# Performance work log

Measured on AMD Instinct MI355X. Metric: run time of the kernel, lower is better.

## Reference

```python
import jax, jax.numpy as jnp
import numpy as np

B, N, DIM = 4, 2048, 512
HEADS, DIM_HEAD = 8, 64
INNER = HEADS * DIM_HEAD  # 512
EPS = 1e-5
SCALE = DIM_HEAD ** -0.5


def _layernorm(x, g):
    # matches custom LayerNorm: unbiased=False var, no bias term
    mean = jnp.mean(x, axis=-1, keepdims=True)
    var = jnp.var(x, axis=-1, keepdims=True)
    return (x - mean) * jax.lax.rsqrt(var + EPS) * g


def setup_inputs() -> dict:
    key = jax.random.key(0)
    ks = jax.random.split(key, 6)
    x = jax.random.normal(ks[0], (B, N, DIM), dtype=jnp.float32)
    attn_bias = jax.random.normal(ks[1], (HEADS, N, N), dtype=jnp.float32)
    w_q = jax.random.normal(ks[2], (DIM, INNER), dtype=jnp.float32) * 0.02
    w_kv = jax.random.normal(ks[3], (DIM, 2 * DIM_HEAD), dtype=jnp.float32) * 0.02
    w_out = jax.random.normal(ks[4], (INNER, DIM), dtype=jnp.float32) * 0.02
    g_in = jnp.ones((DIM,), dtype=jnp.float32)
    g_out = jnp.ones((DIM,), dtype=jnp.float32)
    return {"x": x, "attn_bias": attn_bias, "w_q": w_q, "w_kv": w_kv,
            "w_out": w_out, "g_in": g_in, "g_out": g_out}


def reference(x, attn_bias, w_q, w_kv, w_out, g_in, g_out):
    b, n, _ = x.shape
    xn = _layernorm(x, g_in)                                  # [b, n, dim]
    q = (xn @ w_q).reshape(b, n, HEADS, DIM_HEAD)
    q = jnp.transpose(q, (0, 2, 1, 3)) * SCALE                # [b, h, n, d]
    kv = xn @ w_kv                                            # [b, n, 2d]
    k, v = jnp.split(kv, 2, axis=-1)                          # each [b, n, d] (multi-query)
    sim = jnp.einsum('bhid,bjd->bhij', q, k) + attn_bias      # [b, h, n, n]
    attn = jax.nn.softmax(sim, axis=-1)
    out = jnp.einsum('bhij,bjd->bhid', attn, v)               # [b, h, n, d]
    out = jnp.transpose(out, (0, 2, 1, 3)).reshape(b, n, INNER)
    out = out @ w_out                                         # [b, n, dim]
    return _layernorm(out, g_out)
```

## Files before the change

### kernel.cpp

```cpp
#include <hip/hip_runtime.h>
#include <hip/hip_bf16.h>

#define B_ 4
#define N_ 2048
#define DIM_ 512
#define HEADS_ 8
#define DHEAD_ 64
#define EPS_ 1e-5f
#define SCALE_ 0.125f

typedef __attribute__((ext_vector_type(8))) short short8;
typedef __attribute__((ext_vector_type(4))) float f32x4;
#define MFMA16(a, b, c) __builtin_amdgcn_mfma_f32_16x16x32_bf16(a, b, c, 0, 0, 0)

__device__ __forceinline__ float bf2f(__hip_bfloat16 v) { return __bfloat162float(v); }
__device__ __forceinline__ float load_in(const void* p, size_t i, int isf32) {
    if (isf32) return ((const float*)p)[i];
    return bf2f(((const __hip_bfloat16*)p)[i]);
}

__global__ void detect_kernel(const unsigned int* __restrict__ g, int* __restrict__ flag) {
    if (threadIdx.x == 0 && blockIdx.x == 0)
        *flag = (*g == 0x3F800000u) ? 1 : 0;
}

__global__ __launch_bounds__(256) void transpose_w(const void* __restrict__ w,
                                                   __hip_bfloat16* __restrict__ wt,
                                                   int K, int N, const int* __restrict__ flag) {
    int isf32 = *flag;
    int idx = blockIdx.x * 256 + threadIdx.x;
    if (idx >= K * N) return;
    int k = idx / N, n = idx % N;
    wt[(size_t)n * K + k] = __float2bfloat16(load_in(w, idx, isf32));
}

__global__ __launch_bounds__(256) void ln1_kernel(const void* __restrict__ x,
                                                  const void* __restrict__ g,
                                                  __hip_bfloat16* __restrict__ out,
                                                  const int* __restrict__ flag) {
    int isf32 = *flag;
    int row = blockIdx.x;
    int tid = threadIdx.x;
    size_t base = (size_t)row * DIM_;
    float v0 = load_in(x, base + tid, isf32);
    float v1 = load_in(x, base + tid + 256, isf32);
    float s = v0 + v1;
    float sq = v0 * v0 + v1 * v1;
    for (int off = 32; off > 0; off >>= 1) {
        s += __shfl_xor(s, off, 64);
        sq += __shfl_xor(sq, off, 64);
    }
    __shared__ float ls[4], lq[4];
    int wid = tid >> 6;
    if ((tid & 63) == 0) { ls[wid] = s; lq[wid] = sq; }
    __syncthreads();
    s = ls[0] + ls[1] + ls[2] + ls[3];
    sq = lq[0] + lq[1] + lq[2] + lq[3];
    float mean = s * (1.0f / DIM_);
    float var = sq * (1.0f / DIM_) - mean * mean;
    float rstd = rsqrtf(var + EPS_);
    out[base + tid]       = __float2bfloat16((v0 - mean) * rstd * load_in(g, tid, isf32));
    out[base + tid + 256] = __float2bfloat16((v1 - mean) * rstd * load_in(g, tid + 256, isf32));
}

__global__ __launch_bounds__(256) void ln2_kernel(const float* __restrict__ x,
                                                  const void* __restrict__ g,
                                                  void* __restrict__ out,
                                                  const int* __restrict__ flag) {
    int isf32 = *flag;
    int row = blockIdx.x;
    int tid = threadIdx.x;
    const float* xr = x + (size_t)row * DIM_;
    float v0 = xr[tid];
    float v1 = xr[tid + 256];
    float s = v0 + v1;
    float sq = v0 * v0 + v1 * v1;
    for (int off = 32; off > 0; off >>= 1) {
        s += __shfl_xor(s, off, 64);
        sq += __shfl_xor(sq, off, 64);
    }
    __shared__ float ls[4], lq[4];
    int wid = tid >> 6;
    if ((tid & 63) == 0) { ls[wid] = s; lq[wid] = sq; }
    __syncthreads();
    s = ls[0] + ls[1] + ls[2] + ls[3];
    sq = lq[0] + lq[1] + lq[2] + lq[3];
    float mean = s * (1.0f / DIM_);
    float var = sq * (1.0f / DIM_) - mean * mean;
    float rstd = rsqrtf(var + EPS_);
    float r0 = (v0 - mean) * rstd * load_in(g, tid, isf32);
    float r1 = (v1 - mean) * rstd * load_in(g, tid + 256, isf32);
    size_t base = (size_t)row * DIM_;
    if (isf32) {
        ((float*)out)[base + tid] = r0;
        ((float*)out)[base + tid + 256] = r1;
    } else {
        ((__hip_bfloat16*)out)[base + tid] = __float2bfloat16(r0);
        ((__hip_bfloat16*)out)[base + tid + 256] = __float2bfloat16(r1);
    }
}

template <int MODE>
__global__ __launch_bounds__(256) void gemm_mfma(const __hip_bfloat16* __restrict__ A,
                                                 const __hip_bfloat16* __restrict__ Bt,
                                                 void* __restrict__ Cout,
                                                 void* __restrict__ Cout2,
                                                 int M, int N, int K) {
    __shared__ __align__(16) __hip_bfloat16 As[64][72];
    __shared__ __align__(16) __hip_bfloat16 Bs[64][72];
    int tid = threadIdx.x;
    int lane = tid & 63, wave = tid >> 6;
    int quad = lane >> 4, l15 = lane & 15;
    int wr = (wave & 1) * 32, wc = (wave >> 1) * 32;
    int m0 = blockIdx.y * 64, n0 = blockIdx.x * 64;
    f32x4 acc[2][2] = {};

    for (int k0 = 0; k0 < K; k0 += 64) {
        __syncthreads();
#pragma unroll
        for (int t = 0; t < 2; ++t) {
            int idx = tid + 256 * t;
            int r = idx >> 3, cc = (idx & 7) * 8;
            *(uint4*)&As[r][cc] = *(const uint4*)(A + (size_t)(m0 + r) * K + k0 + cc);
            *(uint4*)&Bs[r][cc] = *(const uint4*)(Bt + (size_t)(n0 + r) * K + k0 + cc);
        }
        __syncthreads();
#pragma unroll
        for (int ks = 0; ks < 2; ++ks) {
            short8 a0 = *(const short8*)&As[wr + l15][ks * 32 + quad * 8];
            short8 a1 = *(const short8*)&As[wr + 16 + l15][ks * 32 + quad * 8];
            short8 b0 = *(const short8*)&Bs[wc + l15][ks * 32 + quad * 8];
            short8 b1 = *(const short8*)&Bs[wc + 16 + l15][ks * 32 + quad * 8];
            acc[0][0] = MFMA16(a0, b0, acc[0][0]);
            acc[0][1] = MFMA16(a0, b1, acc[0][1]);
            acc[1][0] = MFMA16(a1, b0, acc[1][0]);
            acc[1][1] = MFMA16(a1, b1, acc[1][1]);
        }
    }
#pragma unroll
    for (int i = 0; i < 2; ++i)
#pragma unroll
        for (int j = 0; j < 2; ++j)
#pragma unroll
            for (int r = 0; r < 4; ++r) {
                int row = m0 + wr + i * 16 + quad * 4 + r;
                int col = n0 + wc + j * 16 + l15;
                float v = acc[i][j][r];
                if (MODE == 0) {
                    ((__hip_bfloat16*)Cout)[(size_t)row * 512 + col] = __float2bfloat16(v * SCALE_);
                } else if (MODE == 1) {
                    if (col < 64)
                        ((__hip_bfloat16*)Cout)[(size_t)row * 64 + col] = __float2bfloat16(v);
                    else
                        ((__hip_bfloat16*)Cout2)[((size_t)((row >> 11) * 64 + (col - 64)) << 11) + (row & 2047)] = __float2bfloat16(v);
                } else {
                    ((float*)Cout)[(size_t)row * N + col] = v;
                }
            }
}

__global__ __launch_bounds__(256) void attn_mfma(const __hip_bfloat16* __restrict__ qb,
                                                 const __hip_bfloat16* __restrict__ kb,
                                                 const __hip_bfloat16* __restrict__ vtb,
                                                 const void* __restrict__ bias,
                                                 __hip_bfloat16* __restrict__ ao,
                                                 const int* __restrict__ flag) {
    int isf32 = *flag;
    __shared__ __align__(16) __hip_bfloat16 Qs[64][72];
    __shared__ __align__(16) __hip_bfloat16 KsPs[128 * 72];
    __shared__ __align__(16) __hip_bfloat16 Vt[64][136];
    __hip_bfloat16(*Ks)[72] = (__hip_bfloat16(*)[72])KsPs;
    __hip_bfloat16(*Ps)[136] = (__hip_bfloat16(*)[136])KsPs;

    int tid = threadIdx.x;
    int lane = tid & 63, wave = tid >> 6;
    int quad = lane >> 4, l15 = lane & 15;
    int q0 = blockIdx.x * 64;
    int h = blockIdx.y, b = blockIdx.z;
    int qr = wave * 16;

#pragma unroll
    for (int t = 0; t < 2; ++t) {
        int idx = tid + 256 * t;
        int r = idx >> 3, cc = (idx & 7) * 8;
        *(uint4*)&Qs[r][cc] = *(const uint4*)(qb + (size_t)(b * N_ + q0 + r) * 512 + h * 64 + cc);
    }
    __syncthreads();
    short8 aQ0 = *(const short8*)&Qs[qr + l15][quad * 8];
    short8 aQ1 = *(const short8*)&Qs[qr + l15][32 + quad * 8];

    float m_i[4], l_i[4];
    f32x4 Oacc[4] = {};
#pragma unroll
    for (int r = 0; r < 4; ++r) { m_i[r] = -INFINITY; l_i[r] = 0.f; }

    const size_t bias_base = (size_t)h * N_ * N_;

    for (int kb_i = 0; kb_i < N_ / 128; ++kb_i) {
        int k0 = kb_i * 128;
        __syncthreads();
#pragma unroll
        for (int t = 0; t < 4; ++t) {
            int idx = tid + 256 * t;
            int r = idx >> 3, cc = (idx & 7) * 8;
            *(uint4*)&Ks[r][cc] = *(const uint4*)(kb + (size_t)(b * N_ + k0 + r) * 64 + cc);
        }
#pragma unroll
        for (int t = 0; t < 4; ++t) {
            int idx = tid + 256 * t;
            int r = idx >> 4, cc = (idx & 15) * 8;
            *(uint4*)&Vt[r][cc] = *(const uint4*)(vtb + ((size_t)(b * 64 + r) << 11) + k0 + cc);
        }
        __syncthreads();

        float bv[8][4];
#pragma unroll
        for (int t = 0; t < 8; ++t)
#pragma unroll
            for (int r = 0; r < 4; ++r)
                bv[t][r] = load_in(bias,
                    bias_base + (size_t)(q0 + qr + quad * 4 + r) * N_ + k0 + t * 16 + l15, isf32);

        f32x4 Sacc[8] = {};
#pragma unroll
        for (int t = 0; t < 8; ++t) {
            short8 b0 = *(const short8*)&Ks[t * 16 + l15][quad * 8];
            short8 b1 = *(const short8*)&Ks[t * 16 + l15][32 + quad * 8];
            Sacc[t] = MFMA16(aQ0, b0, Sacc[t]);
            Sacc[t] = MFMA16(aQ1, b1, Sacc[t]);
        }

        float S[8][4];
#pragma unroll
        for (int t = 0; t < 8; ++t)
#pragma unroll
            for (int r = 0; r < 4; ++r)
                S[t][r] = Sacc[t][r] + bv[t][r];

        float rm[4], mnew[4], alpha[4], rs[4];
#pragma unroll
        for (int r = 0; r < 4; ++r) {
            rm[r] = S[0][r];
#pragma unroll
            for (int t = 1; t < 8; ++t) rm[r] = fmaxf(rm[r], S[t][r]);
        }
#pragma unroll
        for (int mask = 1; mask < 16; mask <<= 1)
#pragma unroll
            for (int r = 0; r < 4; ++r) rm[r] = fmaxf(rm[r], __shfl_xor(rm[r], mask, 64));
#pragma unroll
        for (int r = 0; r < 4; ++r) {
            mnew[r] = fmaxf(m_i[r], rm[r]);
            rs[r] = 0.f;
#pragma unroll
            for (int t = 0; t < 8; ++t) {
                S[t][r] = __expf(S[t][r] - mnew[r]);
                rs[r] += S[t][r];
            }
        }
#pragma unroll
        for (int mask = 1; mask < 16; mask <<= 1)
#pragma unroll
            for (int r = 0; r < 4; ++r) rs[r] += __shfl_xor(rs[r], mask, 64);
#pragma unroll
        for (int r = 0; r < 4; ++r) {
            alpha[r] = __expf(m_i[r] - mnew[r]);
            l_i[r] = l_i[r] * alpha[r] + rs[r];
            m_i[r] = mnew[r];
#pragma unroll
            for (int d = 0; d < 4; ++d) Oacc[d][r] *= alpha[r];
        }

        __syncthreads();
#pragma unroll
        for (int t = 0; t < 8; ++t)
#pragma unroll
            for (int r = 0; r < 4; ++r)
                Ps[qr + quad * 4 + r][t * 16 + l15] = __float2bfloat16(S[t][r]);

#pragma unroll
        for (int ks = 0; ks < 4; ++ks) {
            short8 aP = *(const short8*)&Ps[qr + l15][ks * 32 + quad * 8];
#pragma unroll
            for (int d = 0; d < 4; ++d) {
                short8 bV = *(const short8*)&Vt[d * 16 + l15][ks * 32 + quad * 8];
                Oacc[d] = MFMA16(aP, bV, Oacc[d]);
            }
        }
    }

#pragma unroll
    for (int d = 0; d < 4; ++d)
#pragma unroll
        for (int r = 0; r < 4; ++r) {
            float v = Oacc[d][r] / l_i[r];
            ao[(size_t)(b * N_ + q0 + qr + quad * 4 + r) * 512 + h * 64 + d * 16 + l15] =
                __float2bfloat16(v);
        }
}

extern "C" void kernel_launch(void* const* d_in, const int* in_sizes, int n_in,
                              void* d_out, int out_size, void* d_ws, size_t ws_size,
                              hipStream_t stream) {
    const void* x         = d_in[0];
    const void* attn_bias = d_in[1];
    const void* w_q       = d_in[2];
    const void* w_kv      = d_in[3];
    const void* w_out     = d_in[4];
    const void* g_in      = d_in[5];
    const void* g_out     = d_in[6];

    char* w = (char*)d_ws;
    __hip_bfloat16* xn   = (__hip_bfloat16*)w;
    __hip_bfloat16* qsc  = (__hip_bfloat16*)(w + (8u << 20));
    __hip_bfloat16* ao   = (__hip_bfloat16*)(w + (16u << 20));
    __hip_bfloat16* kbuf = (__hip_bfloat16*)(w + (24u << 20));
    __hip_bfloat16* vtb  = (__hip_bfloat16*)(w + (25u << 20));
    __hip_bfloat16* wqT  = (__hip_bfloat16*)(w + (26u << 20));
    __hip_bfloat16* wkvT = (__hip_bfloat16*)(w + (26u << 20) + 524288);
    __hip_bfloat16* woT  = (__hip_bfloat16*)(w + (26u << 20) + 524288 + 131072);
    int* flag            = (int*)(w + (26u << 20) + 524288 + 131072 + 524288);
    float* pj            = (float*)w;

    const int R = B_ * N_;

    hipLaunchKernelGGL(detect_kernel, dim3(1), dim3(1), 0, stream,
                       (const unsigned int*)g_in, flag);
    hipLaunchKernelGGL(transpose_w, dim3(512 * 512 / 256), dim3(256), 0, stream,
                       w_q, wqT, 512, 512, flag);
    hipLaunchKernelGGL(transpose_w, dim3(512 * 128 / 256), dim3(256), 0, stream,
                       w_kv, wkvT, 512, 128, flag);
    hipLaunchKernelGGL(transpose_w, dim3(512 * 512 / 256), dim3(256), 0, stream,
                       w_out, woT, 512, 512, flag);
    hipLaunchKernelGGL(ln1_kernel, dim3(R), dim3(256), 0, stream, x, g_in, xn, flag);
    hipLaunchKernelGGL(HIP_KERNEL_NAME(gemm_mfma<0>), dim3(512 / 64, R / 64), dim3(256), 0, stream,
                       xn, wqT, (void*)qsc, nullptr, R, 512, 512);
    hipLaunchKernelGGL(HIP_KERNEL_NAME(gemm_mfma<1>), dim3(128 / 64, R / 64), dim3(256), 0, stream,
                       xn, wkvT, (void*)kbuf, (void*)vtb, R, 128, 512);
    hipLaunchKernelGGL(attn_mfma, dim3(N_ / 64, HEADS_, B_), dim3(256), 0, stream,
                       qsc, kbuf, vtb, attn_bias, ao, flag);
    hipLaunchKernelGGL(HIP_KERNEL_NAME(gemm_mfma<2>), dim3(512 / 64, R / 64), dim3(256), 0, stream,
                       ao, woT, (void*)pj, nullptr, R, 512, 512);
    hipLaunchKernelGGL(ln2_kernel, dim3(R), dim3(256), 0, stream, pj, g_out, d_out, flag);
}
```

Before: 383.5 us.

## Transpose QK^T MFMA for row-per-lane softmax and use 128x128 GEMM tiles

Swaps the operands of the QK^T MFMA so each lane holds one query row across four consecutive keys. Row max and sum then need only two cross-lane shuffles, and the attention bias loads become float4 or ushort4 vector loads instead of scalar strided loads. P is written to shared memory as packed 4-wide stores. The Q and output projection GEMMs move to a 128x128 tile kernel with a 4x4 MFMA block per wave for more register reuse, at the cost of fewer blocks and higher register pressure.

```diff
diff --git a/kernel.cpp b/kernel.cpp
--- a/kernel.cpp
+++ b/kernel.cpp
@@ -14,6 +14,9 @@
 #define MFMA16(a, b, c) __builtin_amdgcn_mfma_f32_16x16x32_bf16(a, b, c, 0, 0, 0)
 
 __device__ __forceinline__ float bf2f(__hip_bfloat16 v) { return __bfloat162float(v); }
+__device__ __forceinline__ float us2f(unsigned short u) {
+    __hip_bfloat16 h; *(unsigned short*)&h = u; return bf2f(h);
+}
 __device__ __forceinline__ float load_in(const void* p, size_t i, int isf32) {
     if (isf32) return ((const float*)p)[i];
     return bf2f(((const __hip_bfloat16*)p)[i]);
@@ -100,12 +103,11 @@
     }
 }
 
-template <int MODE>
-__global__ __launch_bounds__(256) void gemm_mfma(const __hip_bfloat16* __restrict__ A,
-                                                 const __hip_bfloat16* __restrict__ Bt,
-                                                 void* __restrict__ Cout,
-                                                 void* __restrict__ Cout2,
-                                                 int M, int N, int K) {
+__global__ __launch_bounds__(256) void gemm_mfma_kv(const __hip_bfloat16* __restrict__ A,
+                                                    const __hip_bfloat16* __restrict__ Bt,
+                                                    __hip_bfloat16* __restrict__ Kout,
+                                                    __hip_bfloat16* __restrict__ VTout,
+                                                    int M, int N, int K) {
     __shared__ __align__(16) __hip_bfloat16 As[64][72];
     __shared__ __align__(16) __hip_bfloat16 Bs[64][72];
     int tid = threadIdx.x;
@@ -146,16 +148,65 @@
                 int row = m0 + wr + i * 16 + quad * 4 + r;
                 int col = n0 + wc + j * 16 + l15;
                 float v = acc[i][j][r];
-                if (MODE == 0) {
-                    ((__hip_bfloat16*)Cout)[(size_t)row * 512 + col] = __float2bfloat16(v * SCALE_);
-                } else if (MODE == 1) {
-                    if (col < 64)
-                        ((__hip_bfloat16*)Cout)[(size_t)row * 64 + col] = __float2bfloat16(v);
-                    else
-                        ((__hip_bfloat16*)Cout2)[((size_t)((row >> 11) * 64 + (col - 64)) << 11) + (row & 2047)] = __float2bfloat16(v);
-                } else {
+                if (col < 64)
+                    Kout[(size_t)row * 64 + col] = __float2bfloat16(v);
+                else
+                    VTout[((size_t)((row >> 11) * 64 + (col - 64)) << 11) + (row & 2047)] = __float2bfloat16(v);
+            }
+}
+
+template <int MODE>
+__global__ __launch_bounds__(256) void gemm_mfma128(const __hip_bfloat16* __restrict__ A,
+                                                    const __hip_bfloat16* __restrict__ Bt,
+                                                    void* __restrict__ Cout,
+                                                    int M, int N, int K) {
+    __shared__ __align__(16) __hip_bfloat16 As[128][72];
+    __shared__ __align__(16) __hip_bfloat16 Bs[128][72];
+    int tid = threadIdx.x;
+    int lane = tid & 63, wave = tid >> 6;
+    int quad = lane >> 4, l15 = lane & 15;
+    int wr = (wave & 1) * 64, wc = (wave >> 1) * 64;
+    int m0 = blockIdx.y * 128, n0 = blockIdx.x * 128;
+    f32x4 acc[4][4] = {};
+
+    for (int k0 = 0; k0 < K; k0 += 64) {
+        __syncthreads();
+#pragma unroll
+        for (int t = 0; t < 4; ++t) {
+            int idx = tid + 256 * t;
+            int r = idx >> 3, cc = (idx & 7) * 8;
+            *(uint4*)&As[r][cc] = *(const uint4*)(A + (size_t)(m0 + r) * K + k0 + cc);
+            *(uint4*)&Bs[r][cc] = *(const uint4*)(Bt + (size_t)(n0 + r) * K + k0 + cc);
+        }
+        __syncthreads();
+#pragma unroll
+        for (int ks = 0; ks < 2; ++ks) {
+            short8 a[4], b[4];
+#pragma unroll
+            for (int i = 0; i < 4; ++i) {
+                a[i] = *(const short8*)&As[wr + i * 16 + l15][ks * 32 + quad * 8];
+                b[i] = *(const short8*)&Bs[wc + i * 16 + l15][ks * 32 + quad * 8];
+            }
+#pragma unroll
+            for (int i = 0; i < 4; ++i)
+#pragma unroll
+                for (int j = 0; j < 4; ++j)
+                    acc[i][j] = MFMA16(a[i], b[j], acc[i][j]);
+        }
+    }
+#pragma unroll
+    for (int i = 0; i < 4; ++i)
+#pragma unroll
+        for (int j = 0; j < 4; ++j)
+#pragma unroll
+            for (int r = 0; r < 4; ++r) {
+                int row = m0 + wr + i * 16 + quad * 4 + r;
+                int col = n0 + wc + j * 16 + l15;
+                float v = acc[i][j][r];
+                if (MODE == 0)
+                    ((__hip_bfloat16*)Cout)[(size_t)row * N + col] = __float2bfloat16(v * SCALE_);
+                else
                     ((float*)Cout)[(size_t)row * N + col] = v;
-                }
             }
 }
 
@@ -189,12 +240,11 @@
     short8 aQ0 = *(const short8*)&Qs[qr + l15][quad * 8];
     short8 aQ1 = *(const short8*)&Qs[qr + l15][32 + quad * 8];
 
-    float m_i[4], l_i[4];
+    float m_i = -INFINITY, l_i = 0.f;
     f32x4 Oacc[4] = {};
-#pragma unroll
-    for (int r = 0; r < 4; ++r) { m_i[r] = -INFINITY; l_i[r] = 0.f; }
-
-    const size_t bias_base = (size_t)h * N_ * N_;
+
+    const char* biasp = (const char*)bias;
+    const size_t brow = (size_t)h * N_ * N_ + (size_t)(q0 + qr + l15) * N_;
 
     for (int kb_i = 0; kb_i < N_ / 128; ++kb_i) {
         int k0 = kb_i * 128;
@@ -215,68 +265,73 @@
 
         float bv[8][4];
 #pragma unroll
+        for (int t = 0; t < 8; ++t) {
+            size_t eoff = brow + k0 + t * 16 + quad * 4;
+            if (isf32) {
+                float4 f = *(const float4*)(biasp + eoff * 4);
+                bv[t][0] = f.x; bv[t][1] = f.y; bv[t][2] = f.z; bv[t][3] = f.w;
+            } else {
+                ushort4 u = *(const ushort4*)(biasp + eoff * 2);
+                bv[t][0] = us2f(u.x); bv[t][1] = us2f(u.y);
+                bv[t][2] = us2f(u.z); bv[t][3] = us2f(u.w);
+            }
+        }
+
+        f32x4 Sacc[8] = {};
+#pragma unroll
+        for (int t = 0; t < 8; ++t) {
+            short8 k0f = *(const short8*)&Ks[t * 16 + l15][quad * 8];
+            short8 k1f = *(const short8*)&Ks[t * 16 + l15][32 + quad * 8];
+            Sacc[t] = MFMA16(k0f, aQ0, Sacc[t]);
+            Sacc[t] = MFMA16(k1f, aQ1, Sacc[t]);
+        }
+
+        float S[8][4];
+        float rm = -INFINITY;
+#pragma unroll
         for (int t = 0; t < 8; ++t)
 #pragma unroll
-            for (int r = 0; r < 4; ++r)
-                bv[t][r] = load_in(bias,
-                    bias_base + (size_t)(q0 + qr + quad * 4 + r) * N_ + k0 + t * 16 + l15, isf32);
-
-        f32x4 Sacc[8] = {};
+            for (int r = 0; r < 4; ++r) {
+                S[t][r] = Sacc[t][r] + bv[t][r];
+                rm = fmaxf(rm, S[t][r]);
+            }
+        rm = fmaxf(rm, __shfl_xor(rm, 16, 64));
+        rm = fmaxf(rm, __shfl_xor(rm, 32, 64));
+        float mnew = fmaxf(m_i, rm);
+        float rs = 0.f;
+#pragma unroll
+        for (int t = 0; t < 8; ++t)
+#pragma unroll
+            for (int r = 0; r < 4; ++r) {
+                S[t][r] = __expf(S[t][r] - mnew);
+                rs += S[t][r];
+            }
+        rs += __shfl_xor(rs, 16, 64);
+        rs += __shfl_xor(rs, 32, 64);
+        float alpha = __expf(m_i - mnew);
+        l_i = l_i * alpha + rs;
+        m_i = mnew;
+
+        float al[4];
+#pragma unroll
+        for (int r = 0; r < 4; ++r) al[r] = __shfl(alpha, quad * 4 + r, 64);
+#pragma unroll
+        for (int d = 0; d < 4; ++d)
+#pragma unroll
+            for (int r = 0; r < 4; ++r) Oacc[d][r] *= al[r];
+
+        __syncthreads();
 #pragma unroll
         for (int t = 0; t < 8; ++t) {
-            short8 b0 = *(const short8*)&Ks[t * 16 + l15][quad * 8];
-            short8 b1 = *(const short8*)&Ks[t * 16 + l15][32 + quad * 8];
-            Sacc[t] = MFMA16(aQ0, b0, Sacc[t]);
-            Sacc[t] = MFMA16(aQ1, b1, Sacc[t]);
-        }
-
-        float S[8][4];
-#pragma unroll
-        for (int t = 0; t < 8; ++t)
-#pragma unroll
-            for (int r = 0; r < 4; ++r)
-                S[t][r] = Sacc[t][r] + bv[t][r];
-
-        float rm[4], mnew[4], alpha[4], rs[4];
-#pragma unroll
-        for (int r = 0; r < 4; ++r) {
-            rm[r] = S[0][r];
-#pragma unroll
-            for (int t = 1; t < 8; ++t) rm[r] = fmaxf(rm[r], S[t][r]);
-        }
-#pragma unroll
-        for (int mask = 1; mask < 16; mask <<= 1)
-#pragma unroll
-            for (int r = 0; r < 4; ++r) rm[r] = fmaxf(rm[r], __shfl_xor(rm[r], mask, 64));
-#pragma unroll
-        for (int r = 0; r < 4; ++r) {
-            mnew[r] = fmaxf(m_i[r], rm[r]);
-            rs[r] = 0.f;
-#pragma unroll
-            for (int t = 0; t < 8; ++t) {
-                S[t][r] = __expf(S[t][r] - mnew[r]);
-                rs[r] += S[t][r];
-            }
-        }
-#pragma unroll
-        for (int mask = 1; mask < 16; mask <<= 1)
-#pragma unroll
-            for (int r = 0; r < 4; ++r) rs[r] += __shfl_xor(rs[r], mask, 64);
-#pragma unroll
-        for (int r = 0; r < 4; ++r) {
-            alpha[r] = __expf(m_i[r] - mnew[r]);
-            l_i[r] = l_i[r] * alpha[r] + rs[r];
-            m_i[r] = mnew[r];
-#pragma unroll
-            for (int d = 0; d < 4; ++d) Oacc[d][r] *= alpha[r];
-        }
-
-        __syncthreads();
-#pragma unroll
-        for (int t = 0; t < 8; ++t)
-#pragma unroll
-            for (int r = 0; r < 4; ++r)
-                Ps[qr + quad * 4 + r][t * 16 + l15] = __float2bfloat16(S[t][r]);
+            ushort4 u;
+            __hip_bfloat16 h0 = __float2bfloat16(S[t][0]);
+            __hip_bfloat16 h1 = __float2bfloat16(S[t][1]);
+            __hip_bfloat16 h2 = __float2bfloat16(S[t][2]);
+            __hip_bfloat16 h3 = __float2bfloat16(S[t][3]);
+            u.x = *(unsigned short*)&h0; u.y = *(unsigned short*)&h1;
+            u.z = *(unsigned short*)&h2; u.w = *(unsigned short*)&h3;
+            *(ushort4*)&Ps[qr + l15][t * 16 + quad * 4] = u;
+        }
 
 #pragma unroll
         for (int ks = 0; ks < 4; ++ks) {
@@ -289,11 +344,14 @@
         }
     }
 
+    float li[4];
+#pragma unroll
+    for (int r = 0; r < 4; ++r) li[r] = __shfl(l_i, quad * 4 + r, 64);
 #pragma unroll
     for (int d = 0; d < 4; ++d)
 #pragma unroll
         for (int r = 0; r < 4; ++r) {
-            float v = Oacc[d][r] / l_i[r];
+            float v = Oacc[d][r] / li[r];
             ao[(size_t)(b * N_ + q0 + qr + quad * 4 + r) * 512 + h * 64 + d * 16 + l15] =
                 __float2bfloat16(v);
         }
@@ -333,13 +391,13 @@
     hipLaunchKernelGGL(transpose_w, dim3(512 * 512 / 256), dim3(256), 0, stream,
                        w_out, woT, 512, 512, flag);
     hipLaunchKernelGGL(ln1_kernel, dim3(R), dim3(256), 0, stream, x, g_in, xn, flag);
-    hipLaunchKernelGGL(HIP_KERNEL_NAME(gemm_mfma<0>), dim3(512 / 64, R / 64), dim3(256), 0, stream,
-                       xn, wqT, (void*)qsc, nullptr, R, 512, 512);
-    hipLaunchKernelGGL(HIP_KERNEL_NAME(gemm_mfma<1>), dim3(128 / 64, R / 64), dim3(256), 0, stream,
-                       xn, wkvT, (void*)kbuf, (void*)vtb, R, 128, 512);
+    hipLaunchKernelGGL(HIP_KERNEL_NAME(gemm_mfma128<0>), dim3(512 / 128, R / 128), dim3(256), 0, stream,
+                       xn, wqT, (void*)qsc, R, 512, 512);
+    hipLaunchKernelGGL(gemm_mfma_kv, dim3(128 / 64, R / 64), dim3(256), 0, stream,
+                       xn, wkvT, kbuf, vtb, R, 128, 512);
     hipLaunchKernelGGL(attn_mfma, dim3(N_ / 64, HEADS_, B_), dim3(256), 0, stream,
                        qsc, kbuf, vtb, attn_bias, ao, flag);
-    hipLaunchKernelGGL(HIP_KERNEL_NAME(gemm_mfma<2>), dim3(512 / 64, R / 64), dim3(256), 0, stream,
-                       ao, woT, (void*)pj, nullptr, R, 512, 512);
+    hipLaunchKernelGGL(HIP_KERNEL_NAME(gemm_mfma128<2>), dim3(512 / 128, R / 128), dim3(256), 0, stream,
+                       ao, woT, (void*)pj, R, 512, 512);
     hipLaunchKernelGGL(ln2_kernel, dim3(R), dim3(256), 0, stream, pj, g_out, d_out, flag);
 }
```

After: 359.9 us. 1.07x faster.
